# Performance work log

Measured on AMD Instinct MI355X. Metric: run time of the kernel, lower is better.

Reference implementation:

```python
import jax, jax.numpy as jnp
import numpy as np

N_NODES = 50000
N_EDGES = 800000
IN_C, HID_C, OUT_C = 64, 64, 32


def setup_inputs() -> dict:
    key = jax.random.key(0)
    ks = jax.random.split(key, 8)
    x = jax.random.normal(ks[0], (N_NODES, IN_C), dtype=jnp.float32)
    edge_index = jax.random.randint(ks[1], (2, N_EDGES), 0, N_NODES, dtype=jnp.int64)
    s1 = 1.0 / np.sqrt(IN_C)
    s2 = 1.0 / np.sqrt(HID_C)
    W_rel1 = jax.random.uniform(ks[2], (IN_C, HID_C), jnp.float32, -s1, s1)
    W_root1 = jax.random.uniform(ks[3], (IN_C, HID_C), jnp.float32, -s1, s1)
    b1 = jax.random.uniform(ks[4], (HID_C,), jnp.float32, -s1, s1)
    W_rel2 = jax.random.uniform(ks[5], (HID_C, OUT_C), jnp.float32, -s2, s2)
    W_root2 = jax.random.uniform(ks[6], (HID_C, OUT_C), jnp.float32, -s2, s2)
    b2 = jax.random.uniform(ks[7], (OUT_C,), jnp.float32, -s2, s2)
    return {"x": x, "edge_index": edge_index, "W_rel1": W_rel1, "W_root1": W_root1,
            "b1": b1, "W_rel2": W_rel2, "W_root2": W_root2, "b2": b2}


def _graph_conv(x, src, dst, W_rel, W_root, b):
    # aggregate neighbor features (sum over incoming edges), then linear
    agg = jax.ops.segment_sum(x[src], dst, num_segments=N_NODES)  # [N, C_in]
    return agg @ W_rel + x @ W_root + b


def reference(x, edge_index, W_rel1, W_root1, b1, W_rel2, W_root2, b2):
    src, dst = edge_index[0], edge_index[1]
    h = jax.nn.relu(_graph_conv(x, src, dst, W_rel1, W_root1, b1))
    out = _graph_conv(h, src, dst, W_rel2, W_root2, b2)
    return out
```

## Files before the change

kernel.cpp:

```cpp
#include <hip/hip_runtime.h>

static constexpr int N_NODES = 50000;
static constexpr int N_EDGES = 800000;

static constexpr int NBK      = 98;
static constexpr int BCAP     = 10240;
static constexpr int MAXE     = BCAP / 512;
static constexpr int BIN_TILE = 2048;
static constexpr int BIN_BLOCKS = (N_EDGES + BIN_TILE - 1) / BIN_TILE;
static constexpr int PRE1_TILES  = (N_NODES + 15) / 16;
static constexpr int PRE1_BLOCKS = (PRE1_TILES + 3) / 4;

typedef __attribute__((ext_vector_type(8))) short   bf16x8;
typedef __attribute__((ext_vector_type(4))) float   floatx4;

__device__ __forceinline__ unsigned short f2b(float f) {
    union { float f; unsigned u; } v; v.f = f;
    unsigned r = v.u + 0x7FFFu + ((v.u >> 16) & 1u);
    return (unsigned short)(r >> 16);
}
__device__ __forceinline__ float blo(unsigned v) {
    union { unsigned u; float f; } c; c.u = v << 16; return c.f;
}
__device__ __forceinline__ float bhi(unsigned v) {
    union { unsigned u; float f; } c; c.u = v & 0xffff0000u; return c.f;
}
__device__ __forceinline__ unsigned pk2(float a, float b) {
    return (unsigned)f2b(a) | ((unsigned)f2b(b) << 16);
}

__device__ __forceinline__ void bin_body(
    int bb, const int* __restrict__ srcv, const int* __restrict__ dstv,
    int* __restrict__ bcnt, unsigned* __restrict__ epair)
{
    __shared__ uint2 stage[BIN_TILE];
    __shared__ int cnt[128];
    __shared__ int scn[128];
    __shared__ int pref[NBK];
    __shared__ int gbase[NBK];

    int tid   = threadIdx.x;
    int base  = bb * BIN_TILE;
    int tileN = min(BIN_TILE, N_EDGES - base);

    if (tid < 128) cnt[tid] = 0;
    __syncthreads();

    int ss[8], dd[8], sl[8];
#pragma unroll
    for (int j = 0; j < 8; ++j) {
        int i = tid + j * 256;
        ss[j] = -1; dd[j] = 0; sl[j] = 0;
        if (i < tileN) {
            ss[j] = srcv[base + i];
            dd[j] = dstv[base + i];
            sl[j] = atomicAdd(&cnt[dd[j] >> 9], 1);
        }
    }
    __syncthreads();

    int own = (tid < 128) ? cnt[tid] : 0;
    if (tid < 128) scn[tid] = own;
    __syncthreads();
    for (int off = 1; off < 128; off <<= 1) {
        int t = 0;
        if (tid < 128 && tid >= off) t = scn[tid - off];
        __syncthreads();
        if (tid < 128) scn[tid] += t;
        __syncthreads();
    }
    if (tid < NBK) {
        pref[tid]  = scn[tid] - cnt[tid];
        gbase[tid] = tid * BCAP + atomicAdd(&bcnt[tid], cnt[tid]);
    }
    __syncthreads();

#pragma unroll
    for (int j = 0; j < 8; ++j) {
        if (ss[j] >= 0) {
            int b = dd[j] >> 9;
            stage[pref[b] + sl[j]] = uint2{(unsigned)ss[j], (unsigned)dd[j]};
        }
    }
    __syncthreads();

    for (int i = tid; i < tileN; i += 256) {
        uint2 pd = stage[i];
        int b = (int)(pd.y >> 9);
        epair[(size_t)gbase[b] + (i - pref[b])] = (pd.x << 9) | (pd.y & 511u);
    }
}

__device__ __forceinline__ void pre1_body(
    int bb, const float* __restrict__ x,
    const float* __restrict__ Wrel, const float* __restrict__ Wroot,
    const float* __restrict__ bias,
    unsigned short* __restrict__ u1, unsigned short* __restrict__ r1)
{
    int lane = threadIdx.x & 63;
    int c15  = lane & 15;
    int q    = lane >> 4;

    bf16x8 bf[2][4][2];
#pragma unroll
    for (int mat = 0; mat < 2; ++mat) {
        const float* W = mat ? Wroot : Wrel;
#pragma unroll
        for (int ct = 0; ct < 4; ++ct) {
            int c = ct * 16 + c15;
#pragma unroll
            for (int kf = 0; kf < 2; ++kf) {
                int kb = kf * 32 + q * 8;
                bf16x8 f;
#pragma unroll
                for (int j = 0; j < 8; ++j)
                    f[j] = (short)f2b(W[(kb + j) * 64 + c]);
                bf[mat][ct][kf] = f;
            }
        }
    }
    float bv[4];
#pragma unroll
    for (int ct = 0; ct < 4; ++ct) bv[ct] = bias[ct * 16 + c15];

    int tile = bb * 4 + (threadIdx.x >> 6);
    if (tile * 16 >= N_NODES) return;
    int row0 = tile * 16;

    const float* xr = x + (size_t)(row0 + c15) * 64;
    bf16x8 a0, a1;
#pragma unroll
    for (int j = 0; j < 8; ++j) {
        a0[j] = (short)f2b(xr[q * 8 + j]);
        a1[j] = (short)f2b(xr[32 + q * 8 + j]);
    }

    floatx4 z = {0.f, 0.f, 0.f, 0.f};
    floatx4 acc[2][4];
#pragma unroll
    for (int mat = 0; mat < 2; ++mat)
#pragma unroll
        for (int ct = 0; ct < 4; ++ct) {
            floatx4 a = __builtin_amdgcn_mfma_f32_16x16x32_bf16(a0, bf[mat][ct][0], z, 0, 0, 0);
            acc[mat][ct] = __builtin_amdgcn_mfma_f32_16x16x32_bf16(a1, bf[mat][ct][1], a, 0, 0, 0);
        }

#pragma unroll
    for (int reg = 0; reg < 4; ++reg) {
        int row = row0 + q * 4 + reg;
        uint2 uu, rr;
        uu.x = pk2(acc[0][0][reg],          acc[0][1][reg]);
        uu.y = pk2(acc[0][2][reg],          acc[0][3][reg]);
        rr.x = pk2(acc[1][0][reg] + bv[0],  acc[1][1][reg] + bv[1]);
        rr.y = pk2(acc[1][2][reg] + bv[2],  acc[1][3][reg] + bv[3]);
        *reinterpret_cast<uint2*>(u1 + (size_t)row * 64 + c15 * 4) = uu;
        *reinterpret_cast<uint2*>(r1 + (size_t)row * 64 + c15 * 4) = rr;
    }
}

__global__ __launch_bounds__(256) void k_binpre1(
    const int* __restrict__ srcv, const int* __restrict__ dstv,
    int* __restrict__ bcnt, unsigned* __restrict__ epair,
    const float* __restrict__ x,
    const float* __restrict__ Wrel, const float* __restrict__ Wroot,
    const float* __restrict__ bias,
    unsigned short* __restrict__ u1, unsigned short* __restrict__ r1)
{
    if ((int)blockIdx.x < BIN_BLOCKS)
        bin_body(blockIdx.x, srcv, dstv, bcnt, epair);
    else
        pre1_body(blockIdx.x - BIN_BLOCKS, x, Wrel, Wroot, bias, u1, r1);
}

__global__ __launch_bounds__(512) void k_build(
    const unsigned* __restrict__ epair, const int* __restrict__ bcnt,
    int* __restrict__ offsets, int* __restrict__ esrc)
{
    __shared__ int cnt[512];
    __shared__ int scn[512];
    __shared__ int start[512];
    __shared__ int s_base;

    int b = blockIdx.x;
    int t = threadIdx.x;
    int node0 = b << 9;
    int ncnt  = min(512, N_NODES - node0);
    int beg   = b * BCAP;
    int m     = bcnt[b];

    cnt[t] = 0;
    __syncthreads();

    unsigned ev[MAXE]; int sl[MAXE];
#pragma unroll
    for (int j = 0; j < MAXE; ++j) {
        int i = t + j * 512;
        ev[j] = 0; sl[j] = -1;
        if (i < m) {
            ev[j] = epair[beg + i];
            sl[j] = atomicAdd(&cnt[ev[j] & 511u], 1);
        }
    }

    if (t < 64) {
        int m0 = (t      < NBK) ? bcnt[t]      : 0;
        int m1 = (t + 64 < NBK) ? bcnt[t + 64] : 0;
        int pre = ((t < b) ? m0 : 0) + ((t + 64 < b) ? m1 : 0);
        for (int off = 1; off < 64; off <<= 1) pre += __shfl_xor(pre, off);
        if (t == 0) s_base = pre;
    }
    __syncthreads();

    int own = cnt[t];
    scn[t] = own;
    __syncthreads();
    for (int off = 1; off < 512; off <<= 1) {
        int v = (t >= off) ? scn[t - off] : 0;
        __syncthreads();
        scn[t] += v;
        __syncthreads();
    }
    int st = s_base + scn[t] - own;
    start[t] = st;
    if (t < ncnt) offsets[node0 + t] = st;
    if (b == 0 && t == 0) offsets[N_NODES] = N_EDGES;
    __syncthreads();

#pragma unroll
    for (int j = 0; j < MAXE; ++j) {
        if (sl[j] >= 0)
            esrc[start[ev[j] & 511u] + sl[j]] = (int)(ev[j] >> 9);
    }
}

__global__ __launch_bounds__(256) void k_agg64(
    const unsigned short* __restrict__ u1,
    const unsigned short* __restrict__ r1,
    const int* __restrict__ offsets, const int* __restrict__ esrc,
    unsigned short* __restrict__ h)
{
    int lane = threadIdx.x & 63;
    int node = (blockIdx.x * blockDim.x + threadIdx.x) >> 6;
    if (node >= N_NODES) return;
    int j    = lane & 7;
    int slot = lane >> 3;
    int beg = offsets[node], end = offsets[node + 1];
    float s0 = 0.f, s1 = 0.f, s2 = 0.f, s3 = 0.f;
    float s4 = 0.f, s5 = 0.f, s6 = 0.f, s7 = 0.f;
    for (int e = beg + slot; e < end; e += 8) {
        int sv = esrc[e];
        uint4 v = *reinterpret_cast<const uint4*>(u1 + (size_t)sv * 64 + j * 8);
        s0 += blo(v.x); s1 += bhi(v.x);
        s2 += blo(v.y); s3 += bhi(v.y);
        s4 += blo(v.z); s5 += bhi(v.z);
        s6 += blo(v.w); s7 += bhi(v.w);
    }
    s0 += __shfl_xor(s0, 32); s1 += __shfl_xor(s1, 32);
    s2 += __shfl_xor(s2, 32); s3 += __shfl_xor(s3, 32);
    s4 += __shfl_xor(s4, 32); s5 += __shfl_xor(s5, 32);
    s6 += __shfl_xor(s6, 32); s7 += __shfl_xor(s7, 32);
    s0 += __shfl_xor(s0, 16); s1 += __shfl_xor(s1, 16);
    s2 += __shfl_xor(s2, 16); s3 += __shfl_xor(s3, 16);
    s4 += __shfl_xor(s4, 16); s5 += __shfl_xor(s5, 16);
    s6 += __shfl_xor(s6, 16); s7 += __shfl_xor(s7, 16);
    s0 += __shfl_xor(s0, 8);  s1 += __shfl_xor(s1, 8);
    s2 += __shfl_xor(s2, 8);  s3 += __shfl_xor(s3, 8);
    s4 += __shfl_xor(s4, 8);  s5 += __shfl_xor(s5, 8);
    s6 += __shfl_xor(s6, 8);  s7 += __shfl_xor(s7, 8);
    if (lane < 8) {
        uint4 rv = *reinterpret_cast<const uint4*>(r1 + (size_t)node * 64 + j * 8);
        float v0 = fmaxf(s0 + blo(rv.x), 0.f);
        float v1 = fmaxf(s1 + bhi(rv.x), 0.f);
        float v2 = fmaxf(s2 + blo(rv.y), 0.f);
        float v3 = fmaxf(s3 + bhi(rv.y), 0.f);
        float v4 = fmaxf(s4 + blo(rv.z), 0.f);
        float v5 = fmaxf(s5 + bhi(rv.z), 0.f);
        float v6 = fmaxf(s6 + blo(rv.w), 0.f);
        float v7 = fmaxf(s7 + bhi(rv.w), 0.f);
        uint4 o;
        o.x = pk2(v0, v1); o.y = pk2(v2, v3);
        o.z = pk2(v4, v5); o.w = pk2(v6, v7);
        *reinterpret_cast<uint4*>(h + (size_t)node * 64 + j * 8) = o;
    }
}

__global__ __launch_bounds__(256) void k_pre2(
    const unsigned short* __restrict__ h,
    const float* __restrict__ Wrel,
    const float* __restrict__ Wroot,
    const float* __restrict__ bias,
    unsigned short* __restrict__ u2,
    unsigned short* __restrict__ r2)
{
    int lane = threadIdx.x & 63;
    int c15  = lane & 15;
    int q    = lane >> 4;

    bf16x8 bf[2][2][2];
#pragma unroll
    for (int mat = 0; mat < 2; ++mat) {
        const float* W = mat ? Wroot : Wrel;
#pragma unroll
        for (int ct = 0; ct < 2; ++ct) {
            int c = ct * 16 + c15;
#pragma unroll
            for (int kf = 0; kf < 2; ++kf) {
                bf16x8 f;
#pragma unroll
                for (int j = 0; j < 8; ++j) {
                    int p = kf * 32 + q * 8 + j;
                    int tk = (p & 3) * 16 + (p >> 2);
                    f[j] = (short)f2b(W[tk * 32 + c]);
                }
                bf[mat][ct][kf] = f;
            }
        }
    }
    float bv[2];
#pragma unroll
    for (int ct = 0; ct < 2; ++ct) bv[ct] = bias[ct * 16 + c15];

    int tile = (blockIdx.x * blockDim.x + threadIdx.x) >> 6;
    if (tile * 16 >= N_NODES) return;
    int row0 = tile * 16;

    const unsigned short* hr = h + (size_t)(row0 + c15) * 64;
    bf16x8 a0 = *reinterpret_cast<const bf16x8*>(hr + q * 8);
    bf16x8 a1 = *reinterpret_cast<const bf16x8*>(hr + 32 + q * 8);

    floatx4 z = {0.f, 0.f, 0.f, 0.f};
    floatx4 acc[2][2];
#pragma unroll
    for (int mat = 0; mat < 2; ++mat)
#pragma unroll
        for (int ct = 0; ct < 2; ++ct) {
            floatx4 a = __builtin_amdgcn_mfma_f32_16x16x32_bf16(a0, bf[mat][ct][0], z, 0, 0, 0);
            acc[mat][ct] = __builtin_amdgcn_mfma_f32_16x16x32_bf16(a1, bf[mat][ct][1], a, 0, 0, 0);
        }

#pragma unroll
    for (int reg = 0; reg < 4; ++reg) {
        int row = row0 + q * 4 + reg;
        unsigned uu = pk2(acc[0][0][reg],         acc[0][1][reg]);
        unsigned rr = pk2(acc[1][0][reg] + bv[0], acc[1][1][reg] + bv[1]);
        *reinterpret_cast<unsigned*>(u2 + (size_t)row * 32 + c15 * 2) = uu;
        *reinterpret_cast<unsigned*>(r2 + (size_t)row * 32 + c15 * 2) = rr;
    }
}

__global__ __launch_bounds__(256) void k_agg32(
    const unsigned short* __restrict__ u2,
    const unsigned short* __restrict__ r2,
    const int* __restrict__ offsets, const int* __restrict__ esrc,
    float* __restrict__ out)
{
    int lane = threadIdx.x & 63;
    int node = (blockIdx.x * blockDim.x + threadIdx.x) >> 6;
    if (node >= N_NODES) return;
    int j    = lane & 3;
    int slot = lane >> 2;
    int beg = offsets[node], end = offsets[node + 1];
    float s0 = 0.f, s1 = 0.f, s2 = 0.f, s3 = 0.f;
    float s4 = 0.f, s5 = 0.f, s6 = 0.f, s7 = 0.f;
    for (int e = beg + slot; e < end; e += 16) {
        int sv = esrc[e];
        uint4 v = *reinterpret_cast<const uint4*>(u2 + (size_t)sv * 32 + j * 8);
        s0 += blo(v.x); s1 += bhi(v.x);
        s2 += blo(v.y); s3 += bhi(v.y);
        s4 += blo(v.z); s5 += bhi(v.z);
        s6 += blo(v.w); s7 += bhi(v.w);
    }
    s0 += __shfl_xor(s0, 32); s1 += __shfl_xor(s1, 32);
    s2 += __shfl_xor(s2, 32); s3 += __shfl_xor(s3, 32);
    s4 += __shfl_xor(s4, 32); s5 += __shfl_xor(s5, 32);
    s6 += __shfl_xor(s6, 32); s7 += __shfl_xor(s7, 32);
    s0 += __shfl_xor(s0, 16); s1 += __shfl_xor(s1, 16);
    s2 += __shfl_xor(s2, 16); s3 += __shfl_xor(s3, 16);
    s4 += __shfl_xor(s4, 16); s5 += __shfl_xor(s5, 16);
    s6 += __shfl_xor(s6, 16); s7 += __shfl_xor(s7, 16);
    s0 += __shfl_xor(s0, 8);  s1 += __shfl_xor(s1, 8);
    s2 += __shfl_xor(s2, 8);  s3 += __shfl_xor(s3, 8);
    s4 += __shfl_xor(s4, 8);  s5 += __shfl_xor(s5, 8);
    s6 += __shfl_xor(s6, 8);  s7 += __shfl_xor(s7, 8);
    s0 += __shfl_xor(s0, 4);  s1 += __shfl_xor(s1, 4);
    s2 += __shfl_xor(s2, 4);  s3 += __shfl_xor(s3, 4);
    s4 += __shfl_xor(s4, 4);  s5 += __shfl_xor(s5, 4);
    s6 += __shfl_xor(s6, 4);  s7 += __shfl_xor(s7, 4);
    if (lane < 4) {
        uint4 rv = *reinterpret_cast<const uint4*>(r2 + (size_t)node * 32 + j * 8);
        float4 oA, oB;
        oA.x = s0 + blo(rv.x);  oB.x = s1 + bhi(rv.x);
        oA.y = s2 + blo(rv.y);  oB.y = s3 + bhi(rv.y);
        oA.z = s4 + blo(rv.z);  oB.z = s5 + bhi(rv.z);
        oA.w = s6 + blo(rv.w);  oB.w = s7 + bhi(rv.w);
        *reinterpret_cast<float4*>(out + (size_t)node * 32 + j * 4)      = oA;
        *reinterpret_cast<float4*>(out + (size_t)node * 32 + 16 + j * 4) = oB;
    }
}

extern "C" void kernel_launch(void* const* d_in, const int* in_sizes, int n_in,
                              void* d_out, int out_size, void* d_ws, size_t ws_size,
                              hipStream_t stream) {
    const float* x      = (const float*)d_in[0];
    const int*   ei     = (const int*)  d_in[1];
    const float* Wrel1  = (const float*)d_in[2];
    const float* Wroot1 = (const float*)d_in[3];
    const float* b1     = (const float*)d_in[4];
    const float* Wrel2  = (const float*)d_in[5];
    const float* Wroot2 = (const float*)d_in[6];
    const float* b2     = (const float*)d_in[7];
    float*       out    = (float*)d_out;

    const int* srcv = ei;
    const int* dstv = ei + N_EDGES;

    char* p = (char*)d_ws;
    auto alloc = [&](size_t bytes) {
        char* r = p;
        p += (bytes + 255) & ~(size_t)255;
        return r;
    };
    int*      offsets = (int*)     alloc(sizeof(int) * (N_NODES + 1));
    int*      bcnt    = (int*)     alloc(sizeof(int) * NBK);
    unsigned* epair   = (unsigned*)alloc(sizeof(unsigned) * (size_t)NBK * BCAP);
    int*      esrc    = (int*)     alloc(sizeof(int) * N_EDGES);
    unsigned short* u1 = (unsigned short*)alloc(sizeof(short) * (size_t)N_NODES * 64);
    unsigned short* r1 = (unsigned short*)alloc(sizeof(short) * (size_t)N_NODES * 64);
    unsigned short* h  = (unsigned short*)alloc(sizeof(short) * (size_t)N_NODES * 64);
    unsigned short* u2 = (unsigned short*)alloc(sizeof(short) * (size_t)N_NODES * 32);
    unsigned short* r2 = (unsigned short*)alloc(sizeof(short) * (size_t)N_NODES * 32);

    const int nodeBlocks = (N_NODES * 64 + 255) / 256;
    const int tileBlocks = PRE1_BLOCKS;

    hipMemsetAsync(bcnt, 0, sizeof(int) * NBK, stream);
    k_binpre1<<<BIN_BLOCKS + PRE1_BLOCKS, 256, 0, stream>>>(
        srcv, dstv, bcnt, epair, x, Wrel1, Wroot1, b1, u1, r1);
    k_build<<<NBK, 512, 0, stream>>>(epair, bcnt, offsets, esrc);

    k_agg64<<<nodeBlocks, 256, 0, stream>>>(u1, r1, offsets, esrc, h);

    k_pre2<<<tileBlocks, 256, 0, stream>>>(h, Wrel2, Wroot2, b2, u2, r2);

    k_agg32<<<nodeBlocks, 256, 0, stream>>>(u2, r2, offsets, esrc, out);
}
```

Before: 92.87 us.

## Fuse layer-1 aggregation with layer-2 projection via LDS and halve bucket width

The layer-1 neighbor aggregation and the layer-2 MFMA projection now run in one kernel. Each block aggregates 64 nodes into a swizzled LDS tile and then runs the MFMA, so the h intermediate is never written to or read back from global memory, and one launch is removed. The CSR build also switches to 256-node buckets, giving 196 build blocks instead of 98, for more parallelism in k_build. The cost is that each wave now processes 16 nodes one after another, which lowers parallelism in the aggregation phase and may hurt latency hiding on the gathers.

```diff
diff --git a/kernel.cpp b/kernel.cpp
--- a/kernel.cpp
+++ b/kernel.cpp
@@ -3,8 +3,8 @@
 static constexpr int N_NODES = 50000;
 static constexpr int N_EDGES = 800000;
 
-static constexpr int NBK      = 98;
-static constexpr int BCAP     = 10240;
+static constexpr int NBK      = 196;
+static constexpr int BCAP     = 5120;
 static constexpr int MAXE     = BCAP / 512;
 static constexpr int BIN_TILE = 2048;
 static constexpr int BIN_BLOCKS = (N_EDGES + BIN_TILE - 1) / BIN_TILE;
@@ -34,8 +34,8 @@
     int* __restrict__ bcnt, unsigned* __restrict__ epair)
 {
     __shared__ uint2 stage[BIN_TILE];
-    __shared__ int cnt[128];
-    __shared__ int scn[128];
+    __shared__ int cnt[256];
+    __shared__ int scn[256];
     __shared__ int pref[NBK];
     __shared__ int gbase[NBK];
 
@@ -43,7 +43,7 @@
     int base  = bb * BIN_TILE;
     int tileN = min(BIN_TILE, N_EDGES - base);
 
-    if (tid < 128) cnt[tid] = 0;
+    cnt[tid] = 0;
     __syncthreads();
 
     int ss[8], dd[8], sl[8];
@@ -54,19 +54,18 @@
         if (i < tileN) {
             ss[j] = srcv[base + i];
             dd[j] = dstv[base + i];
-            sl[j] = atomicAdd(&cnt[dd[j] >> 9], 1);
-        }
-    }
-    __syncthreads();
-
-    int own = (tid < 128) ? cnt[tid] : 0;
-    if (tid < 128) scn[tid] = own;
-    __syncthreads();
-    for (int off = 1; off < 128; off <<= 1) {
-        int t = 0;
-        if (tid < 128 && tid >= off) t = scn[tid - off];
+            sl[j] = atomicAdd(&cnt[dd[j] >> 8], 1);
+        }
+    }
+    __syncthreads();
+
+    int own = cnt[tid];
+    scn[tid] = own;
+    __syncthreads();
+    for (int off = 1; off < 256; off <<= 1) {
+        int t = (tid >= off) ? scn[tid - off] : 0;
         __syncthreads();
-        if (tid < 128) scn[tid] += t;
+        scn[tid] += t;
         __syncthreads();
     }
     if (tid < NBK) {
@@ -78,7 +77,7 @@
 #pragma unroll
     for (int j = 0; j < 8; ++j) {
         if (ss[j] >= 0) {
-            int b = dd[j] >> 9;
+            int b = dd[j] >> 8;
             stage[pref[b] + sl[j]] = uint2{(unsigned)ss[j], (unsigned)dd[j]};
         }
     }
@@ -86,8 +85,8 @@
 
     for (int i = tid; i < tileN; i += 256) {
         uint2 pd = stage[i];
-        int b = (int)(pd.y >> 9);
-        epair[(size_t)gbase[b] + (i - pref[b])] = (pd.x << 9) | (pd.y & 511u);
+        int b = (int)(pd.y >> 8);
+        epair[(size_t)gbase[b] + (i - pref[b])] = (pd.x << 8) | (pd.y & 255u);
     }
 }
 
@@ -176,19 +175,19 @@
     const unsigned* __restrict__ epair, const int* __restrict__ bcnt,
     int* __restrict__ offsets, int* __restrict__ esrc)
 {
-    __shared__ int cnt[512];
-    __shared__ int scn[512];
-    __shared__ int start[512];
+    __shared__ int cnt[256];
+    __shared__ int scn[256];
+    __shared__ int start[256];
     __shared__ int s_base;
 
     int b = blockIdx.x;
     int t = threadIdx.x;
-    int node0 = b << 9;
-    int ncnt  = min(512, N_NODES - node0);
+    int node0 = b << 8;
+    int ncnt  = min(256, N_NODES - node0);
     int beg   = b * BCAP;
     int m     = bcnt[b];
 
-    cnt[t] = 0;
+    if (t < 256) cnt[t] = 0;
     __syncthreads();
 
     unsigned ev[MAXE]; int sl[MAXE];
@@ -198,103 +197,115 @@
         ev[j] = 0; sl[j] = -1;
         if (i < m) {
             ev[j] = epair[beg + i];
-            sl[j] = atomicAdd(&cnt[ev[j] & 511u], 1);
+            sl[j] = atomicAdd(&cnt[ev[j] & 255u], 1);
         }
     }
 
     if (t < 64) {
-        int m0 = (t      < NBK) ? bcnt[t]      : 0;
-        int m1 = (t + 64 < NBK) ? bcnt[t + 64] : 0;
-        int pre = ((t < b) ? m0 : 0) + ((t + 64 < b) ? m1 : 0);
+        int pre = 0;
+#pragma unroll
+        for (int k = 0; k < 4; ++k) {
+            int i = t + (k << 6);
+            if (i < b) pre += bcnt[i];
+        }
         for (int off = 1; off < 64; off <<= 1) pre += __shfl_xor(pre, off);
         if (t == 0) s_base = pre;
     }
     __syncthreads();
 
-    int own = cnt[t];
-    scn[t] = own;
-    __syncthreads();
-    for (int off = 1; off < 512; off <<= 1) {
-        int v = (t >= off) ? scn[t - off] : 0;
+    int own = (t < 256) ? cnt[t] : 0;
+    if (t < 256) scn[t] = own;
+    __syncthreads();
+    for (int off = 1; off < 256; off <<= 1) {
+        int v = (t < 256 && t >= off) ? scn[t - off] : 0;
         __syncthreads();
-        scn[t] += v;
+        if (t < 256) scn[t] += v;
         __syncthreads();
     }
-    int st = s_base + scn[t] - own;
-    start[t] = st;
-    if (t < ncnt) offsets[node0 + t] = st;
+    if (t < 256) {
+        int st = s_base + scn[t] - own;
+        start[t] = st;
+        if (t < ncnt) offsets[node0 + t] = st;
+    }
     if (b == 0 && t == 0) offsets[N_NODES] = N_EDGES;
     __syncthreads();
 
 #pragma unroll
     for (int j = 0; j < MAXE; ++j) {
         if (sl[j] >= 0)
-            esrc[start[ev[j] & 511u] + sl[j]] = (int)(ev[j] >> 9);
-    }
-}
-
-__global__ __launch_bounds__(256) void k_agg64(
+            esrc[start[ev[j] & 255u] + sl[j]] = (int)(ev[j] >> 8);
+    }
+}
+
+__global__ __launch_bounds__(256) void k_aggp2(
     const unsigned short* __restrict__ u1,
     const unsigned short* __restrict__ r1,
     const int* __restrict__ offsets, const int* __restrict__ esrc,
-    unsigned short* __restrict__ h)
-{
-    int lane = threadIdx.x & 63;
-    int node = (blockIdx.x * blockDim.x + threadIdx.x) >> 6;
-    if (node >= N_NODES) return;
-    int j    = lane & 7;
-    int slot = lane >> 3;
-    int beg = offsets[node], end = offsets[node + 1];
-    float s0 = 0.f, s1 = 0.f, s2 = 0.f, s3 = 0.f;
-    float s4 = 0.f, s5 = 0.f, s6 = 0.f, s7 = 0.f;
-    for (int e = beg + slot; e < end; e += 8) {
-        int sv = esrc[e];
-        uint4 v = *reinterpret_cast<const uint4*>(u1 + (size_t)sv * 64 + j * 8);
-        s0 += blo(v.x); s1 += bhi(v.x);
-        s2 += blo(v.y); s3 += bhi(v.y);
-        s4 += blo(v.z); s5 += bhi(v.z);
-        s6 += blo(v.w); s7 += bhi(v.w);
-    }
-    s0 += __shfl_xor(s0, 32); s1 += __shfl_xor(s1, 32);
-    s2 += __shfl_xor(s2, 32); s3 += __shfl_xor(s3, 32);
-    s4 += __shfl_xor(s4, 32); s5 += __shfl_xor(s5, 32);
-    s6 += __shfl_xor(s6, 32); s7 += __shfl_xor(s7, 32);
-    s0 += __shfl_xor(s0, 16); s1 += __shfl_xor(s1, 16);
-    s2 += __shfl_xor(s2, 16); s3 += __shfl_xor(s3, 16);
-    s4 += __shfl_xor(s4, 16); s5 += __shfl_xor(s5, 16);
-    s6 += __shfl_xor(s6, 16); s7 += __shfl_xor(s7, 16);
-    s0 += __shfl_xor(s0, 8);  s1 += __shfl_xor(s1, 8);
-    s2 += __shfl_xor(s2, 8);  s3 += __shfl_xor(s3, 8);
-    s4 += __shfl_xor(s4, 8);  s5 += __shfl_xor(s5, 8);
-    s6 += __shfl_xor(s6, 8);  s7 += __shfl_xor(s7, 8);
-    if (lane < 8) {
-        uint4 rv = *reinterpret_cast<const uint4*>(r1 + (size_t)node * 64 + j * 8);
-        float v0 = fmaxf(s0 + blo(rv.x), 0.f);
-        float v1 = fmaxf(s1 + bhi(rv.x), 0.f);
-        float v2 = fmaxf(s2 + blo(rv.y), 0.f);
-        float v3 = fmaxf(s3 + bhi(rv.y), 0.f);
-        float v4 = fmaxf(s4 + blo(rv.z), 0.f);
-        float v5 = fmaxf(s5 + bhi(rv.z), 0.f);
-        float v6 = fmaxf(s6 + blo(rv.w), 0.f);
-        float v7 = fmaxf(s7 + bhi(rv.w), 0.f);
-        uint4 o;
-        o.x = pk2(v0, v1); o.y = pk2(v2, v3);
-        o.z = pk2(v4, v5); o.w = pk2(v6, v7);
-        *reinterpret_cast<uint4*>(h + (size_t)node * 64 + j * 8) = o;
-    }
-}
-
-__global__ __launch_bounds__(256) void k_pre2(
-    const unsigned short* __restrict__ h,
     const float* __restrict__ Wrel,
     const float* __restrict__ Wroot,
     const float* __restrict__ bias,
     unsigned short* __restrict__ u2,
     unsigned short* __restrict__ r2)
 {
+    __shared__ unsigned short hlds[64 * 64];
+
+    int w    = threadIdx.x >> 6;
     int lane = threadIdx.x & 63;
-    int c15  = lane & 15;
-    int q    = lane >> 4;
+    int j    = lane & 7;
+    int slot = lane >> 3;
+
+    for (int t = 0; t < 16; ++t) {
+        int nl   = w * 16 + t;
+        int node = blockIdx.x * 64 + nl;
+        if (node < N_NODES) {
+            int beg = offsets[node], end = offsets[node + 1];
+            float s0 = 0.f, s1 = 0.f, s2 = 0.f, s3 = 0.f;
+            float s4 = 0.f, s5 = 0.f, s6 = 0.f, s7 = 0.f;
+            for (int e = beg + slot; e < end; e += 8) {
+                int sv = esrc[e];
+                uint4 v = *reinterpret_cast<const uint4*>(u1 + (size_t)sv * 64 + j * 8);
+                s0 += blo(v.x); s1 += bhi(v.x);
+                s2 += blo(v.y); s3 += bhi(v.y);
+                s4 += blo(v.z); s5 += bhi(v.z);
+                s6 += blo(v.w); s7 += bhi(v.w);
+            }
+            s0 += __shfl_xor(s0, 32); s1 += __shfl_xor(s1, 32);
+            s2 += __shfl_xor(s2, 32); s3 += __shfl_xor(s3, 32);
+            s4 += __shfl_xor(s4, 32); s5 += __shfl_xor(s5, 32);
+            s6 += __shfl_xor(s6, 32); s7 += __shfl_xor(s7, 32);
+            s0 += __shfl_xor(s0, 16); s1 += __shfl_xor(s1, 16);
+            s2 += __shfl_xor(s2, 16); s3 += __shfl_xor(s3, 16);
+            s4 += __shfl_xor(s4, 16); s5 += __shfl_xor(s5, 16);
+            s6 += __shfl_xor(s6, 16); s7 += __shfl_xor(s7, 16);
+            s0 += __shfl_xor(s0, 8);  s1 += __shfl_xor(s1, 8);
+            s2 += __shfl_xor(s2, 8);  s3 += __shfl_xor(s3, 8);
+            s4 += __shfl_xor(s4, 8);  s5 += __shfl_xor(s5, 8);
+            s6 += __shfl_xor(s6, 8);  s7 += __shfl_xor(s7, 8);
+            if (lane < 8) {
+                uint4 rv = *reinterpret_cast<const uint4*>(r1 + (size_t)node * 64 + j * 8);
+                float v0 = fmaxf(s0 + blo(rv.x), 0.f);
+                float v1 = fmaxf(s1 + bhi(rv.x), 0.f);
+                float v2 = fmaxf(s2 + blo(rv.y), 0.f);
+                float v3 = fmaxf(s3 + bhi(rv.y), 0.f);
+                float v4 = fmaxf(s4 + blo(rv.z), 0.f);
+                float v5 = fmaxf(s5 + bhi(rv.z), 0.f);
+                float v6 = fmaxf(s6 + blo(rv.w), 0.f);
+                float v7 = fmaxf(s7 + bhi(rv.w), 0.f);
+                uint4 o;
+                o.x = pk2(v0, v1); o.y = pk2(v2, v3);
+                o.z = pk2(v4, v5); o.w = pk2(v6, v7);
+                unsigned byte = (unsigned)nl * 128u + (((unsigned)j * 16u) ^ (((unsigned)nl & 7u) << 4));
+                *reinterpret_cast<uint4*>((char*)hlds + byte) = o;
+            }
+        }
+    }
+    __syncthreads();
+
+    int c15 = lane & 15;
+    int q   = lane >> 4;
+    int row0l = w * 16;
+    int row0  = blockIdx.x * 64 + row0l;
+    if (row0 >= N_NODES) return;
 
     bf16x8 bf[2][2][2];
 #pragma unroll
@@ -307,10 +318,10 @@
             for (int kf = 0; kf < 2; ++kf) {
                 bf16x8 f;
 #pragma unroll
-                for (int j = 0; j < 8; ++j) {
-                    int p = kf * 32 + q * 8 + j;
+                for (int jj = 0; jj < 8; ++jj) {
+                    int p = kf * 32 + q * 8 + jj;
                     int tk = (p & 3) * 16 + (p >> 2);
-                    f[j] = (short)f2b(W[tk * 32 + c]);
+                    f[jj] = (short)f2b(W[tk * 32 + c]);
                 }
                 bf[mat][ct][kf] = f;
             }
@@ -320,13 +331,10 @@
 #pragma unroll
     for (int ct = 0; ct < 2; ++ct) bv[ct] = bias[ct * 16 + c15];
 
-    int tile = (blockIdx.x * blockDim.x + threadIdx.x) >> 6;
-    if (tile * 16 >= N_NODES) return;
-    int row0 = tile * 16;
-
-    const unsigned short* hr = h + (size_t)(row0 + c15) * 64;
-    bf16x8 a0 = *reinterpret_cast<const bf16x8*>(hr + q * 8);
-    bf16x8 a1 = *reinterpret_cast<const bf16x8*>(hr + 32 + q * 8);
+    int r = row0l + c15;
+    unsigned sw = ((unsigned)r & 7u) << 4;
+    bf16x8 a0 = *reinterpret_cast<const bf16x8*>((char*)hlds + (unsigned)r * 128u + (((unsigned)q * 16u) ^ sw));
+    bf16x8 a1 = *reinterpret_cast<const bf16x8*>((char*)hlds + (unsigned)r * 128u + ((((unsigned)q + 4u) * 16u) ^ sw));
 
     floatx4 z = {0.f, 0.f, 0.f, 0.f};
     floatx4 acc[2][2];
@@ -426,21 +434,19 @@
     int*      esrc    = (int*)     alloc(sizeof(int) * N_EDGES);
     unsigned short* u1 = (unsigned short*)alloc(sizeof(short) * (size_t)N_NODES * 64);
     unsigned short* r1 = (unsigned short*)alloc(sizeof(short) * (size_t)N_NODES * 64);
-    unsigned short* h  = (unsigned short*)alloc(sizeof(short) * (size_t)N_NODES * 64);
     unsigned short* u2 = (unsigned short*)alloc(sizeof(short) * (size_t)N_NODES * 32);
     unsigned short* r2 = (unsigned short*)alloc(sizeof(short) * (size_t)N_NODES * 32);
 
     const int nodeBlocks = (N_NODES * 64 + 255) / 256;
-    const int tileBlocks = PRE1_BLOCKS;
+    const int aggBlocks  = (N_NODES + 63) / 64;
 
     hipMemsetAsync(bcnt, 0, sizeof(int) * NBK, stream);
     k_binpre1<<<BIN_BLOCKS + PRE1_BLOCKS, 256, 0, stream>>>(
         srcv, dstv, bcnt, epair, x, Wrel1, Wroot1, b1, u1, r1);
     k_build<<<NBK, 512, 0, stream>>>(epair, bcnt, offsets, esrc);
 
-    k_agg64<<<nodeBlocks, 256, 0, stream>>>(u1, r1, offsets, esrc, h);
-
-    k_pre2<<<tileBlocks, 256, 0, stream>>>(h, Wrel2, Wroot2, b2, u2, r2);
+    k_aggp2<<<aggBlocks, 256, 0, stream>>>(u1, r1, offsets, esrc,
+                                           Wrel2, Wroot2, b2, u2, r2);
 
     k_agg32<<<nodeBlocks, 256, 0, stream>>>(u2, r2, offsets, esrc, out);
 }
```

Result: slower. 103.2 us (+11.1%).
